# Performance work log

Measured on AMD Instinct MI355X. Metric: run time of the kernel, lower is better.

## Reference

```python
import jax, jax.numpy as jnp
import numpy as np
from jax import lax

B, S, Q, A, L = 8192, 8192, 64, 1024, 3
H = 64  # post-processor hidden


def setup_inputs() -> dict:
    key = jax.random.key(0)
    ks = jax.random.split(key, 9)
    state = jax.random.normal(ks[0], (B, S), dtype=jnp.float32)
    enc_w = jax.random.normal(ks[1], (Q, S), dtype=jnp.float32) * (1.0 / np.sqrt(S))
    enc_b = jnp.zeros((Q,), dtype=jnp.float32)
    quantum_params = jax.random.normal(ks[2], (L, Q, 3), dtype=jnp.float32) * 0.1
    measurement_ops = jax.random.normal(ks[3], (A, Q, 2), dtype=jnp.float32) * 0.1
    w1 = jax.random.normal(ks[4], (H, A), dtype=jnp.float32) * (1.0 / np.sqrt(A))
    b1 = jnp.zeros((H,), dtype=jnp.float32)
    w2 = jax.random.normal(ks[5], (A, H), dtype=jnp.float32) * (1.0 / np.sqrt(H))
    b2 = jnp.zeros((A,), dtype=jnp.float32)
    return {"state": state, "enc_w": enc_w, "enc_b": enc_b,
            "quantum_params": quantum_params, "measurement_ops": measurement_ops,
            "w1": w1, "b1": b1, "w2": w2, "b2": b2}


def reference(state, enc_w, enc_b, quantum_params, measurement_ops, w1, b1, w2, b2):
    # Encode: Linear + softmax. quantum_state = complex(encoded, 0); since every
    # rotation is a real scaling (qs*cos + roll(qs)*sin), the imaginary part
    # stays identically zero, so we track only the real component.
    encoded = jax.nn.softmax(state @ enc_w.T + enc_b, axis=-1)  # [B, Q]

    # Rotation gates applied sequentially in layer -> qubit -> (x,y,z) order,
    # which is exactly the row-major flattening of quantum_params.
    thetas = quantum_params.reshape(-1)  # [L*Q*3]

    def gate(qs, theta):
        c = jnp.cos(theta * 0.5)
        s = jnp.sin(theta * 0.5)
        return qs * c + jnp.roll(qs, 1, axis=-1) * s, None

    qs, _ = lax.scan(gate, encoded, thetas)  # [B, Q]

    # Measurement: torch.sum has no dim -> reduces over batch AND qubit dims.
    # imag == 0, so the ops[:, :, 1] term contributes nothing.
    measurements = jnp.einsum('bq,aq->a', qs, measurement_ops[:, :, 0])  # [A]

    # Post-processor MLP on the [A] vector.
    h = jax.nn.relu(measurements @ w1.T + b1)
    return h @ w2.T + b2  # [A]
```

## Files before the change

### kernel.cpp

```cpp
#include <hip/hip_runtime.h>
#include <hip/hip_fp16.h>

typedef __fp16 h2_t __attribute__((ext_vector_type(2)));
typedef _Float16 f16x8 __attribute__((ext_vector_type(8)));
typedef float f32x4 __attribute__((ext_vector_type(4)));
typedef unsigned int uint32;

#define S_DIM 8192
#define B_DIM 8192
#define Q_DIM 64
#define A_DIM 1024
#define H_DIM 64
#define N_GATES 576

#define MT 64
#define KSPLIT 8
#define KC (S_DIM / KSPLIT)
#define BK 64
#define NSTEP (KC / BK)
#define NCHUNK 4
#define CHUNK (N_GATES / NCHUNK)

__device__ __forceinline__ uint32 pk_f16(float x, float y) {
    h2_t h = __builtin_amdgcn_cvt_pkrtz(x, y);
    return __builtin_bit_cast(uint32, h);
}

__device__ __forceinline__ f32x4 mfma16(uint4 a, uint4 b, f32x4 c) {
    return __builtin_amdgcn_mfma_f32_16x16x32_f16(
        __builtin_bit_cast(f16x8, a), __builtin_bit_cast(f16x8, b), c, 0, 0, 0);
}

__global__ void k_pre(const float* __restrict__ encw, uint4* __restrict__ bpack,
                      const float* __restrict__ w1, const float* __restrict__ mo,
                      float* __restrict__ WM) {
    const int bid = blockIdx.x;
    const int t   = threadIdx.x;
    if (bid < 256) {
        const int gid  = bid * 256 + t;
        const int lane = gid & 63;
        const int nt   = (gid >> 6) & 3;
        const int kt   = gid >> 8;
        const int n = nt * 16 + (lane & 15);
        const int k = kt * 32 + (lane >> 4) * 8;
        const float* p = encw + (size_t)n * S_DIM + k;
        float4 x0 = *(const float4*)p;
        float4 x1 = *(const float4*)(p + 4);
        uint4 r;
        r.x = pk_f16(x0.x, x0.y);
        r.y = pk_f16(x0.z, x0.w);
        r.z = pk_f16(x1.x, x1.y);
        r.w = pk_f16(x1.z, x1.w);
        bpack[gid] = r;
    } else {
        __shared__ float red[4][64];
        const int j    = bid - 256;
        const int lane = t & 63;
        const int wv   = t >> 6;
        const float* w1r = w1 + (size_t)j * A_DIM + wv * 256;
        const float* mop = mo + (size_t)wv * 256 * 128 + lane * 2;
        float acc = 0.f;
        for (int a = 0; a < 256; ++a)
            acc = fmaf(w1r[a], mop[(size_t)a * 128], acc);
        red[wv][lane] = acc;
        __syncthreads();
        if (t < 64)
            WM[(size_t)j * 64 + t] = red[0][t] + red[1][t] + red[2][t] + red[3][t];
    }
}

__global__ __launch_bounds__(256, 4) void k_gemm(
        const float* __restrict__ state, const uint4* __restrict__ bpack,
        float* __restrict__ partial) {
    __shared__ __align__(16) uint32 As[2][MT][36];
    const int t  = threadIdx.x;
    const int w  = t >> 6;
    const int l  = t & 63;
    const int m0 = blockIdx.x * MT;
    const int ks = blockIdx.y;
    const int k0 = ks * KC;

    const int ar = t >> 2;
    const int ac = (t & 3) * 16;
    const float* pa = state + (size_t)(m0 + ar) * S_DIM + k0 + ac;
    const uint4* pb = bpack + (size_t)(k0 >> 5) * 4 * 64 + l;

    const int frow = w * 16 + (l & 15);
    const int fc   = (l >> 4) * 4;

    f32x4 acc[4] = {};
    float4 ra0, ra1, ra2, ra3;
#define LOADA(off) do { \
        const float* p_ = pa + (off); \
        ra0 = *(const float4*)(p_);      ra1 = *(const float4*)(p_ + 4); \
        ra2 = *(const float4*)(p_ + 8);  ra3 = *(const float4*)(p_ + 12); } while (0)

#define CVTWRITE(buf) do { \
        uint4 w0, w1; \
        w0.x = pk_f16(ra0.x, ra0.y); w0.y = pk_f16(ra0.z, ra0.w); \
        w0.z = pk_f16(ra1.x, ra1.y); w0.w = pk_f16(ra1.z, ra1.w); \
        w1.x = pk_f16(ra2.x, ra2.y); w1.y = pk_f16(ra2.z, ra2.w); \
        w1.z = pk_f16(ra3.x, ra3.y); w1.w = pk_f16(ra3.z, ra3.w); \
        *(uint4*)&As[buf][ar][ac >> 1]       = w0; \
        *(uint4*)&As[buf][ar][(ac >> 1) + 4] = w1; } while (0)

    LOADA(0);
    CVTWRITE(0);

    for (int s = 0; s < NSTEP; ++s) {
        const int cur = s & 1;
        if (s + 1 < NSTEP) LOADA((s + 1) * BK);
        uint4 bf0[4], bf1[4];
#pragma unroll
        for (int nt = 0; nt < 4; ++nt) {
            bf0[nt] = pb[(size_t)((s * 2 + 0) * 4 + nt) * 64];
            bf1[nt] = pb[(size_t)((s * 2 + 1) * 4 + nt) * 64];
        }
        __syncthreads();
        uint4 af0 = *(const uint4*)&As[cur][frow][fc];
        uint4 af1 = *(const uint4*)&As[cur][frow][fc + 16];
#pragma unroll
        for (int nt = 0; nt < 4; ++nt) {
            acc[nt] = mfma16(af0, bf0[nt], acc[nt]);
            acc[nt] = mfma16(af1, bf1[nt], acc[nt]);
        }
        __syncthreads();
        if (s + 1 < NSTEP) CVTWRITE(cur ^ 1);
    }

    float* pc = partial + (size_t)ks * (B_DIM * Q_DIM);
    const int mr = m0 + w * 16 + (l >> 4) * 4;
    const int nc = l & 15;
#pragma unroll
    for (int nt = 0; nt < 4; ++nt)
#pragma unroll
        for (int r = 0; r < 4; ++r)
            pc[(size_t)(mr + r) * Q_DIM + nt * 16 + nc] = acc[nt][r];
#undef LOADA
#undef CVTWRITE
}

__global__ void k_softmax(const float* __restrict__ partial,
                          const float* __restrict__ encb,
                          float* __restrict__ colsum_parts) {
    __shared__ float red[4][64];
    const int lane = threadIdx.x & 63;
    const int wv   = threadIdx.x >> 6;
    const float eb = encb[lane];
    float accq = 0.f;
    for (int i = 0; i < 8; ++i) {
        const int r = blockIdx.x * 32 + i * 4 + wv;
        float x = eb;
#pragma unroll
        for (int ks = 0; ks < KSPLIT; ++ks)
            x += partial[(size_t)ks * (B_DIM * Q_DIM) + (size_t)r * Q_DIM + lane];
        float m = x;
        for (int o = 32; o > 0; o >>= 1) m = fmaxf(m, __shfl_xor(m, o));
        float e = __expf(x - m);
        float s = e;
        for (int o = 32; o > 0; o >>= 1) s += __shfl_xor(s, o);
        accq += e / s;
    }
    red[wv][lane] = accq;
    __syncthreads();
    if (threadIdx.x < 64) {
        colsum_parts[blockIdx.x * 64 + lane] =
            red[0][lane] + red[1][lane] + red[2][lane] + red[3][lane];
    }
}

__global__ void k_final(const float* __restrict__ colsum_parts,
                        const float* __restrict__ qp,
                        const float* __restrict__ WM,
                        const float* __restrict__ b1,
                        const float* __restrict__ w2, const float* __restrict__ b2,
                        float* __restrict__ out) {
    __shared__ float red[4][64];
    __shared__ float t0[64];
    __shared__ float cs[N_GATES], ss[N_GATES];
    __shared__ float pA[NCHUNK][64];
    __shared__ float pB[2][64];
    __shared__ float fv[64];
    __shared__ float gv[64];
    __shared__ float hl[64];
    const int t    = threadIdx.x;
    const int lane = t & 63;
    const int wv   = t >> 6;

    for (int g = t; g < N_GATES; g += 256) {
        float th = qp[g] * 0.5f;
        cs[g] = __cosf(th);
        ss[g] = __sinf(th);
    }
    {
        float c = 0.f;
#pragma unroll
        for (int i = 0; i < 64; ++i)
            c += colsum_parts[(size_t)(wv * 64 + i) * 64 + lane];
        red[wv][lane] = c;
    }
    __syncthreads();
    if (t < 64)
        t0[t] = red[0][t] + red[1][t] + red[2][t] + red[3][t];
    {
        float p = (lane == 0) ? 1.f : 0.f;
        const int g0 = wv * CHUNK;
        for (int g = 0; g < CHUNK; ++g) {
            float prev = __shfl(p, (lane + 63) & 63);
            p = fmaf(cs[g0 + g], p, ss[g0 + g] * prev);
        }
        pA[wv][lane] = p;
    }
    __syncthreads();
    if (wv < 2) {
        float r = 0.f;
        for (int i = 0; i < 64; ++i)
            r += pA[2 * wv][i] * pA[2 * wv + 1][(lane - i) & 63];
        pB[wv][lane] = r;
    }
    __syncthreads();
    if (wv == 0) {
        float r = 0.f;
        for (int i = 0; i < 64; ++i)
            r += pB[0][i] * pB[1][(lane - i) & 63];
        fv[lane] = r;
    }
    __syncthreads();
    if (wv == 0) {
        float r = 0.f;
        for (int i = 0; i < 64; ++i)
            r += fv[i] * t0[(lane - i) & 63];
        gv[lane] = r;
    }
    __syncthreads();
    if (t < 64) {
        float v = 0.f;
        const float* wr = WM + (size_t)t * 64;
#pragma unroll
        for (int q = 0; q < 64; ++q)
            v = fmaf(wr[q], gv[q], v);
        hl[t] = fmaxf(v + b1[t], 0.f);
    }
    __syncthreads();
    const int a = blockIdx.x * 4 + wv;
    float v = w2[(size_t)a * H_DIM + lane] * hl[lane];
    for (int o = 32; o > 0; o >>= 1) v += __shfl_xor(v, o);
    if (lane == 0) out[a] = v + b2[a];
}

extern "C" void kernel_launch(void* const* d_in, const int* in_sizes, int n_in,
                              void* d_out, int out_size, void* d_ws, size_t ws_size,
                              hipStream_t stream) {
    const float* state = (const float*)d_in[0];
    const float* encw  = (const float*)d_in[1];
    const float* encb  = (const float*)d_in[2];
    const float* qp    = (const float*)d_in[3];
    const float* mo    = (const float*)d_in[4];
    const float* w1    = (const float*)d_in[5];
    const float* b1    = (const float*)d_in[6];
    const float* w2    = (const float*)d_in[7];
    const float* b2    = (const float*)d_in[8];
    float* out = (float*)d_out;

    float* ws           = (float*)d_ws;
    float* colsum_parts = ws;
    float* partial      = ws + 16384;
    float* WM           = partial + (size_t)KSPLIT * B_DIM * Q_DIM;
    uint4* bpack        = (uint4*)(WM + 4096);

    k_pre<<<dim3(320), dim3(256), 0, stream>>>(encw, bpack, w1, mo, WM);
    k_gemm<<<dim3(B_DIM / MT, KSPLIT), dim3(256), 0, stream>>>(state, bpack, partial);
    k_softmax<<<dim3(256), dim3(256), 0, stream>>>(partial, encb, colsum_parts);
    k_final<<<dim3(256), dim3(256), 0, stream>>>(colsum_parts, qp, WM, b1, w2, b2, out);
}
```

Measured before the change: 95.87 us.

## Load GEMM A tiles with direct global-to-LDS DMA and XOR swizzle

Replaces the register-staged fp32 load, f16 convert and LDS write of the state tile with `global_load_lds` DMA that writes raw fp32 directly into a double-buffered, XOR-swizzled LDS tile. The fp32 to f16 conversion moves to after the LDS read. One `__syncthreads` per step is replaced by a manual `vmcnt` wait plus a single barrier. The aim is to cut VGPR pressure and instruction overhead in the bandwidth-bound encoder GEMM and to overlap the next tile's loads better. In exchange, LDS use doubles to 32KB per block, and correctness now depends on the hand-written `vmcnt` count.

After: 95.72 us. No clear change (-0.1%).

```diff
diff --git a/kernel.cpp b/kernel.cpp
--- a/kernel.cpp
+++ b/kernel.cpp
@@ -29,6 +29,12 @@
 __device__ __forceinline__ f32x4 mfma16(uint4 a, uint4 b, f32x4 c) {
     return __builtin_amdgcn_mfma_f32_16x16x32_f16(
         __builtin_bit_cast(f16x8, a), __builtin_bit_cast(f16x8, b), c, 0, 0, 0);
+}
+
+__device__ __forceinline__ void gload_lds16(const float* g, float* lds) {
+    __builtin_amdgcn_global_load_lds(
+        (const __attribute__((address_space(1))) void*)g,
+        (__attribute__((address_space(3))) void*)lds, 16, 0, 0);
 }
 
 __global__ void k_pre(const float* __restrict__ encw, uint4* __restrict__ bpack,
@@ -72,7 +78,7 @@
 __global__ __launch_bounds__(256, 4) void k_gemm(
         const float* __restrict__ state, const uint4* __restrict__ bpack,
         float* __restrict__ partial) {
-    __shared__ __align__(16) uint32 As[2][MT][36];
+    __shared__ __align__(16) float As[2][MT * BK];
     const int t  = threadIdx.x;
     const int w  = t >> 6;
     const int l  = t & 63;
@@ -80,53 +86,54 @@
     const int ks = blockIdx.y;
     const int k0 = ks * KC;
 
-    const int ar = t >> 2;
-    const int ac = (t & 3) * 16;
-    const float* pa = state + (size_t)(m0 + ar) * S_DIM + k0 + ac;
     const uint4* pb = bpack + (size_t)(k0 >> 5) * 4 * 64 + l;
 
-    const int frow = w * 16 + (l & 15);
-    const int fc   = (l >> 4) * 4;
+    const int fr = w * 16 + (l & 15);
+    const int g2 = l >> 4;
+    const int fx = fr & 15;
+
+#define DMA(BUF, S) do { \
+        _Pragma("unroll") \
+        for (int i = 0; i < 4; ++i) { \
+            const int rl = (w * 4 + i) * 4 + (l >> 4); \
+            const int ss = (l & 15) ^ (rl & 15); \
+            const float* gp = state + (size_t)(m0 + rl) * S_DIM + k0 + (S) * BK + ss * 4; \
+            gload_lds16(gp, &As[BUF][(w * 4 + i) * 256]); \
+        } } while (0)
 
     f32x4 acc[4] = {};
-    float4 ra0, ra1, ra2, ra3;
-#define LOADA(off) do { \
-        const float* p_ = pa + (off); \
-        ra0 = *(const float4*)(p_);      ra1 = *(const float4*)(p_ + 4); \
-        ra2 = *(const float4*)(p_ + 8);  ra3 = *(const float4*)(p_ + 12); } while (0)
-
-#define CVTWRITE(buf) do { \
-        uint4 w0, w1; \
-        w0.x = pk_f16(ra0.x, ra0.y); w0.y = pk_f16(ra0.z, ra0.w); \
-        w0.z = pk_f16(ra1.x, ra1.y); w0.w = pk_f16(ra1.z, ra1.w); \
-        w1.x = pk_f16(ra2.x, ra2.y); w1.y = pk_f16(ra2.z, ra2.w); \
-        w1.z = pk_f16(ra3.x, ra3.y); w1.w = pk_f16(ra3.z, ra3.w); \
-        *(uint4*)&As[buf][ar][ac >> 1]       = w0; \
-        *(uint4*)&As[buf][ar][(ac >> 1) + 4] = w1; } while (0)
-
-    LOADA(0);
-    CVTWRITE(0);
+
+    DMA(0, 0);
 
     for (int s = 0; s < NSTEP; ++s) {
         const int cur = s & 1;
-        if (s + 1 < NSTEP) LOADA((s + 1) * BK);
         uint4 bf0[4], bf1[4];
 #pragma unroll
         for (int nt = 0; nt < 4; ++nt) {
             bf0[nt] = pb[(size_t)((s * 2 + 0) * 4 + nt) * 64];
             bf1[nt] = pb[(size_t)((s * 2 + 1) * 4 + nt) * 64];
         }
-        __syncthreads();
-        uint4 af0 = *(const uint4*)&As[cur][frow][fc];
-        uint4 af1 = *(const uint4*)&As[cur][frow][fc + 16];
+        asm volatile("s_waitcnt vmcnt(8)" ::: "memory");
+        __builtin_amdgcn_s_barrier();
+        __builtin_amdgcn_sched_barrier(0);
+        if (s + 1 < NSTEP) DMA(cur ^ 1, s + 1);
+        const int b0 = fr * BK;
+        const float4 f00 = *(const float4*)&As[cur][b0 + (((2 * g2 + 0) ^ fx) << 2)];
+        const float4 f01 = *(const float4*)&As[cur][b0 + (((2 * g2 + 1) ^ fx) << 2)];
+        const float4 f10 = *(const float4*)&As[cur][b0 + (((8 + 2 * g2 + 0) ^ fx) << 2)];
+        const float4 f11 = *(const float4*)&As[cur][b0 + (((8 + 2 * g2 + 1) ^ fx) << 2)];
+        uint4 af0, af1;
+        af0.x = pk_f16(f00.x, f00.y); af0.y = pk_f16(f00.z, f00.w);
+        af0.z = pk_f16(f01.x, f01.y); af0.w = pk_f16(f01.z, f01.w);
+        af1.x = pk_f16(f10.x, f10.y); af1.y = pk_f16(f10.z, f10.w);
+        af1.z = pk_f16(f11.x, f11.y); af1.w = pk_f16(f11.z, f11.w);
 #pragma unroll
         for (int nt = 0; nt < 4; ++nt) {
             acc[nt] = mfma16(af0, bf0[nt], acc[nt]);
             acc[nt] = mfma16(af1, bf1[nt], acc[nt]);
         }
-        __syncthreads();
-        if (s + 1 < NSTEP) CVTWRITE(cur ^ 1);
-    }
+    }
+#undef DMA
 
     float* pc = partial + (size_t)ks * (B_DIM * Q_DIM);
     const int mr = m0 + w * 16 + (l >> 4) * 4;
@@ -136,8 +143,6 @@
 #pragma unroll
         for (int r = 0; r < 4; ++r)
             pc[(size_t)(mr + r) * Q_DIM + nt * 16 + nc] = acc[nt][r];
-#undef LOADA
-#undef CVTWRITE
 }
 
 __global__ void k_softmax(const float* __restrict__ partial,
```
